# Kernel optimization log

Measured on AMD Instinct MI355X. Metric: run time of the kernel, lower is better.

Reference implementation:

```python
import jax, jax.numpy as jnp
import numpy as np

DIM = 512
HID = 4 * DIM
E = 8
B, T = 2, 2048


def setup_inputs() -> dict:
    key = jax.random.key(0)
    ks = jax.random.split(key, 8)
    s = 0.02
    x = jax.random.normal(ks[0], (B, T, DIM), dtype=jnp.float32)
    route = jax.random.randint(ks[1], (B * T,), 0, E, dtype=jnp.int32)
    # stacked per-expert params; Linear y = x @ W + b with W in [in, out] layout
    w_in = jax.random.normal(ks[2], (E, DIM, HID), dtype=jnp.float32) * s
    b_in = jnp.zeros((E, HID), dtype=jnp.float32)
    w_gate = jax.random.normal(ks[3], (E, DIM, HID), dtype=jnp.float32) * s
    b_gate = jnp.zeros((E, HID), dtype=jnp.float32)
    w_out = jax.random.normal(ks[4], (E, HID, DIM), dtype=jnp.float32) * s
    b_out = jnp.zeros((E, DIM), dtype=jnp.float32)
    return {"x": x, "route": route, "w_in": w_in, "b_in": b_in,
            "w_gate": w_gate, "b_gate": b_gate, "w_out": w_out, "b_out": b_out}


def reference(x, route, w_in, b_in, w_gate, b_gate, w_out, b_out):
    Bb, Tt, C = x.shape
    xf = x.reshape(-1, C)  # [N, C]
    out = jnp.zeros_like(xf)
    n_experts = w_in.shape[0]
    # loop over the small fixed expert set; each expert is a SwiGLU FFN,
    # output scattered back by masking (same math as output[idx] += expert(x[idx]))
    for e in range(n_experts):
        mask = (route == e).astype(xf.dtype)[:, None]  # [N, 1]
        h = jax.nn.silu(xf @ w_gate[e] + b_gate[e]) * (xf @ w_in[e] + b_in[e])  # [N, 4C]
        out = out + mask * (h @ w_out[e] + b_out[e])
    return out.reshape(Bb, Tt, C)
```

## Files before the change

kernel.cpp:

```cpp
#include <hip/hip_runtime.h>

#define DIM 512
#define HID 2048
#define NEXP 8

typedef __attribute__((ext_vector_type(8))) short v8s;
typedef __attribute__((ext_vector_type(4))) float v4f;

__device__ __forceinline__ unsigned short f2bf(float f) {
  union { __bf16 b; unsigned short u; } c;
  c.b = (__bf16)f;
  return c.u;
}

__device__ __forceinline__ void gload16(const void* g, void* l) {
  __builtin_amdgcn_global_load_lds(
      (const __attribute__((address_space(1))) unsigned int*)g,
      (__attribute__((address_space(3))) unsigned int*)l, 16, 0, 0);
}

__global__ void route_prep(const int* __restrict__ route, int* __restrict__ meta, int ntok) {
  __shared__ int c[NEXP];
  int t = threadIdx.x;
  if (t < NEXP) c[t] = 0;
  __syncthreads();
  for (int n = t; n < ntok; n += blockDim.x) atomicAdd(&c[route[n]], 1);
  __syncthreads();
  if (t == 0) {
    int acc = 0, pacc = 0;
    for (int e = 0; e < NEXP; ++e) {
      meta[e] = c[e];
      meta[NEXP + e] = acc;
      meta[2 * NEXP + e] = acc;
      meta[3 * NEXP + e] = pacc;
      acc += c[e];
      pacc += ((c[e] + 127) >> 7) << 7;
    }
  }
}

__global__ void fill_perm(const int* __restrict__ route, int* __restrict__ meta,
                          int* __restrict__ perm, int ntok) {
  int n = blockIdx.x * blockDim.x + threadIdx.x;
  if (n < ntok) {
    int p = atomicAdd(&meta[2 * NEXP + route[n]], 1);
    perm[p] = n;
  }
}

__global__ __launch_bounds__(256) void x_conv(
    const float* __restrict__ x, const int* __restrict__ meta,
    const int* __restrict__ perm, unsigned short* __restrict__ xp)
{
  const int bid = blockIdx.x;
  const int e = bid & 7;
  const int mt = bid >> 3;
  const int cnt = meta[e];
  const int padded = ((cnt + 127) >> 7) << 7;
  if (mt * 64 >= padded) return;
  const int off  = meta[NEXP + e];
  const int poff = meta[3 * NEXP + e];
  const int t = threadIdx.x;
  const int r = t & 63, q = t >> 6;
  int arow = mt * 64 + r; if (arow >= cnt) arow = cnt - 1;
  const float* src = x + (size_t)perm[off + arow] * DIM + q * 128;
  unsigned short* dst = xp + (size_t)((poff + mt * 64) >> 6) * 32768;
  #pragma unroll
  for (int j = 0; j < 16; ++j) {
    float4 f0 = ((const float4*)src)[2 * j];
    float4 f1 = ((const float4*)src)[2 * j + 1];
    v8s v;
    v[0] = (short)f2bf(f0.x); v[1] = (short)f2bf(f0.y);
    v[2] = (short)f2bf(f0.z); v[3] = (short)f2bf(f0.w);
    v[4] = (short)f2bf(f1.x); v[5] = (short)f2bf(f1.y);
    v[6] = (short)f2bf(f1.z); v[7] = (short)f2bf(f1.w);
    *(v8s*)(dst + (size_t)((q * 16 + j) * 64 + r) * 8) = v;
  }
}

__global__ __launch_bounds__(256) void wo_conv(
    const float* __restrict__ wo, unsigned short* __restrict__ wop)
{
  const int s = blockIdx.x;
  const int j = blockIdx.y;
  const int e = blockIdx.z;
  const float* src = wo + (size_t)e * HID * DIM;
  unsigned short* dst = wop + (((size_t)e * 8 + j) * 32 + s) * 4096;
  const int t = threadIdx.x;
  #pragma unroll
  for (int i = 0; i < 2; ++i) {
    const int c = t + 256 * i;
    const int kq = c >> 6, n = c & 63;
    const float* srow = src + (size_t)(s * 64 + kq * 8) * DIM + j * 64 + n;
    v8s r;
    #pragma unroll
    for (int q = 0; q < 8; ++q) r[q] = (short)f2bf(srow[(size_t)q * DIM]);
    *(v8s*)(dst + (size_t)c * 8) = r;
  }
}

__global__ __launch_bounds__(256, 2) void gemm1w(
    const unsigned short* __restrict__ xp,
    const float* __restrict__ wg_, const float* __restrict__ bg_,
    const float* __restrict__ wi_, const float* __restrict__ bi_,
    const int* __restrict__ meta,
    unsigned short* __restrict__ hbuf)
{
  const int bid = blockIdx.x;
  const int e = bid >> 6;
  const int j = bid & 63;
  const int cnt = meta[e];
  const int poff = meta[3 * NEXP + e];
  const int n0 = j * 32;

  __shared__ __align__(16) unsigned char lds[81920];

  const int t = threadIdx.x;
  const int l = t & 63, w = t >> 6;
  const int wm = w >> 1, wn = w & 1;
  const int fr = l & 15, fg = l >> 4;

  {
    const int r0 = t >> 1;
    const int h  = t & 1;
    #pragma unroll
    for (int m = 0; m < 2; ++m) {
      const float* src = (m ? wi_ : wg_) + (size_t)e * DIM * HID + n0 + h * 16;
      unsigned char* slab = lds + m * 32768;
      #pragma unroll
      for (int p = 0; p < 4; ++p) {
        const int r = p * 128 + r0;
        const float* row = src + (size_t)r * HID;
        float f[16];
        #pragma unroll
        for (int q = 0; q < 4; ++q) {
          float4 v = ((const float4*)row)[q];
          f[4*q] = v.x; f[4*q+1] = v.y; f[4*q+2] = v.z; f[4*q+3] = v.w;
        }
        unsigned char* dst = slab + ((r >> 3) * 32 + h * 16) * 16 + (r & 7) * 2;
        #pragma unroll
        for (int nn = 0; nn < 16; ++nn)
          *(unsigned short*)(dst + nn * 16) = f2bf(f[nn]);
      }
    }
  }

  const int c = n0 + wn * 16 + fr;
  const float bgv = bg_[(size_t)e * HID + c];
  const float biv = bi_[(size_t)e * HID + c];

  unsigned char* albuf = lds + 65536;
  const int nmt = (cnt + 127) >> 7;

  for (int mt = 0; mt < nmt; ++mt) {
    const int m0 = mt * 128;
    const int tile0 = (poff + m0) >> 6;

    auto stage_a = [&](int s, int b) {
      unsigned char* base = albuf + b * 8192;
      #pragma unroll
      for (int i = 0; i < 2; ++i) {
        const int s_ = t + 256 * i;
        const int kq = s_ >> 7, mr = s_ & 127;
        gload16(xp + (size_t)(tile0 + (mr >> 6)) * 32768 +
                     ((size_t)(s * 4 + kq) * 64 + (mr & 63)) * 8,
                base + s_ * 16);
      }
    };

    stage_a(0, 0);
    __syncthreads();

    v4f aG[4], aI[4];
    #pragma unroll
    for (int i = 0; i < 4; ++i) {
      aG[i] = (v4f){0.f, 0.f, 0.f, 0.f};
      aI[i] = (v4f){0.f, 0.f, 0.f, 0.f};
    }

    int cur = 0;
    for (int s = 0; s < 16; ++s) {
      if (s < 15) stage_a(s + 1, cur ^ 1);
      const unsigned char* base = albuf + cur * 8192;
      v8s af[4], gf, inf;
      #pragma unroll
      for (int mf = 0; mf < 4; ++mf)
        af[mf] = *(const v8s*)(base + (fg * 128 + wm * 64 + mf * 16 + fr) * 16);
      gf  = *(const v8s*)(lds + (((s * 4 + fg) * 32) + wn * 16 + fr) * 16);
      inf = *(const v8s*)(lds + 32768 + (((s * 4 + fg) * 32) + wn * 16 + fr) * 16);
      #pragma unroll
      for (int mf = 0; mf < 4; ++mf) {
        aG[mf] = __builtin_amdgcn_mfma_f32_16x16x32_bf16(af[mf], gf,  aG[mf], 0, 0, 0);
        aI[mf] = __builtin_amdgcn_mfma_f32_16x16x32_bf16(af[mf], inf, aI[mf], 0, 0, 0);
      }
      __syncthreads();
      cur ^= 1;
    }

    #pragma unroll
    for (int mf = 0; mf < 4; ++mf)
      #pragma unroll
      for (int jj = 0; jj < 4; ++jj) {
        const int r = wm * 64 + mf * 16 + fg * 4 + jj;
        const float g = aG[mf][jj] + bgv;
        const float v = aI[mf][jj] + biv;
        const float hval = g / (1.f + __expf(-g)) * v;
        const int grow = poff + m0 + r;
        hbuf[(size_t)(grow >> 6) * 131072 + ((size_t)(c >> 3) * 64 + (grow & 63)) * 8 + (c & 7)] = f2bf(hval);
      }
  }
}

__global__ __launch_bounds__(256, 4) void gemm2g(
    const unsigned short* __restrict__ hbuf,
    const unsigned short* __restrict__ wop, const float* __restrict__ bo_,
    const int* __restrict__ meta, const int* __restrict__ perm,
    float* __restrict__ out)
{
  const int bid = blockIdx.x;
  const int stripe = bid & 63;
  const int mt = bid >> 6;
  const int e = stripe >> 3, jn = stripe & 7;
  const int cnt = meta[e];
  const int m0 = mt * 64;
  if (m0 >= cnt) return;
  const int off = meta[NEXP + e], poff = meta[3 * NEXP + e];
  const int n0 = jn * 64;

  __shared__ __align__(16) unsigned char lds[32768];

  const int t = threadIdx.x;
  const int l = t & 63, w = t >> 6;
  const int wm = w >> 1, wn = w & 1;
  const int fr = l & 15, fg = l >> 4;

  const unsigned short* pa = hbuf + (size_t)((poff + m0) >> 6) * 131072;
  const unsigned short* pb = wop + ((size_t)e * 8 + jn) * 131072;

  v4f acc[2][2];
  #pragma unroll
  for (int i = 0; i < 2; ++i) {
    acc[i][0] = (v4f){0.f, 0.f, 0.f, 0.f};
    acc[i][1] = (v4f){0.f, 0.f, 0.f, 0.f};
  }

  auto stage = [&](int s, int b) {
    unsigned char* base = lds + b * 16384;
    #pragma unroll
    for (int i = 0; i < 2; ++i) {
      const int c = t + 256 * i;
      gload16(pa + (size_t)s * 4096 + (size_t)c * 8, base + c * 16);
      gload16(pb + (size_t)s * 4096 + (size_t)c * 8, base + 8192 + c * 16);
    }
  };

  stage(0, 0);
  __syncthreads();

  int cur = 0;
  for (int s = 0; s < 32; ++s) {
    if (s < 31) stage(s + 1, cur ^ 1);
    const unsigned char* base = lds + cur * 16384;
    #pragma unroll
    for (int kk = 0; kk < 2; ++kk) {
      v8s af[2], bf[2];
      #pragma unroll
      for (int mf = 0; mf < 2; ++mf)
        af[mf] = *(const v8s*)(base + ((kk * 4 + fg) * 64 + wm * 32 + mf * 16 + fr) * 16);
      #pragma unroll
      for (int nf = 0; nf < 2; ++nf)
        bf[nf] = *(const v8s*)(base + 8192 + ((kk * 4 + fg) * 64 + wn * 32 + nf * 16 + fr) * 16);
      #pragma unroll
      for (int mf = 0; mf < 2; ++mf)
        #pragma unroll
        for (int nf = 0; nf < 2; ++nf)
          acc[mf][nf] = __builtin_amdgcn_mfma_f32_16x16x32_bf16(af[mf], bf[nf], acc[mf][nf], 0, 0, 0);
    }
    __syncthreads();
    cur ^= 1;
  }

  #pragma unroll
  for (int nf = 0; nf < 2; ++nf) {
    const int c = n0 + wn * 32 + nf * 16 + fr;
    const float bo = bo_[(size_t)e * DIM + c];
    #pragma unroll
    for (int mf = 0; mf < 2; ++mf)
      #pragma unroll
      for (int jj = 0; jj < 4; ++jj) {
        const int r = wm * 32 + mf * 16 + fg * 4 + jj;
        if (m0 + r < cnt)
          out[(size_t)perm[off + m0 + r] * DIM + c] = acc[mf][nf][jj] + bo;
      }
  }
}

extern "C" void kernel_launch(void* const* d_in, const int* in_sizes, int n_in,
                              void* d_out, int out_size, void* d_ws, size_t ws_size,
                              hipStream_t stream) {
  const float* x      = (const float*)d_in[0];
  const int*   route  = (const int*)d_in[1];
  const float* w_in   = (const float*)d_in[2];
  const float* b_in   = (const float*)d_in[3];
  const float* w_gate = (const float*)d_in[4];
  const float* b_gate = (const float*)d_in[5];
  const float* w_out  = (const float*)d_in[6];
  const float* b_out  = (const float*)d_in[7];
  float* out = (float*)d_out;

  const int ntok = in_sizes[1];

  int* meta = (int*)d_ws;
  int* perm = (int*)((char*)d_ws + 128);

  unsigned short* xp   = (unsigned short*)((char*)d_ws + 65536);
  unsigned short* wop  = (unsigned short*)((char*)d_ws + 65536 + 5242880);
  unsigned short* hbuf = (unsigned short*)((char*)d_ws + 65536 + 5242880 + 16777216);

  const int MT64 = (ntok + 63) / 64;

  route_prep<<<1, 256, 0, stream>>>(route, meta, ntok);
  fill_perm<<<(ntok + 255) / 256, 256, 0, stream>>>(route, meta, perm, ntok);
  x_conv<<<NEXP * MT64, 256, 0, stream>>>(x, meta, perm, xp);
  gemm1w<<<NEXP * 64, 256, 0, stream>>>(
      xp, w_gate, b_gate, w_in, b_in, meta, hbuf);
  wo_conv<<<dim3(32, 8, 8), 256, 0, stream>>>(w_out, wop);
  gemm2g<<<64 * MT64, 256, 0, stream>>>(
      hbuf, wop, b_out, meta, perm, out);
}
```

Measured before the change: 114.0 us.

## Read activation and weight fragments straight from global memory, dropping LDS staging

Both expert GEMMs stop staging the A operand (and in the second GEMM also the weight tile) through double-buffered LDS with async global-to-LDS loads. Instead each wave loads its MFMA fragments directly from global memory. The first GEMM now gives each wave its own 64-row M strip with both 16-column N fragments and no block barriers. The second GEMM uses 32-row by 32-column per-wave tiles with more blocks and higher occupancy. This removes barrier and LDS traffic but depends on L2/cache hit rates and exposes global load latency without explicit prefetch.

```diff
diff --git a/kernel.cpp b/kernel.cpp
--- a/kernel.cpp
+++ b/kernel.cpp
@@ -11,12 +11,6 @@
   union { __bf16 b; unsigned short u; } c;
   c.b = (__bf16)f;
   return c.u;
-}
-
-__device__ __forceinline__ void gload16(const void* g, void* l) {
-  __builtin_amdgcn_global_load_lds(
-      (const __attribute__((address_space(1))) unsigned int*)g,
-      (__attribute__((address_space(3))) unsigned int*)l, 16, 0, 0);
 }
 
 __global__ void route_prep(const int* __restrict__ route, int* __restrict__ meta, int ntok) {
@@ -99,7 +93,7 @@
   }
 }
 
-__global__ __launch_bounds__(256, 2) void gemm1w(
+__global__ __launch_bounds__(256, 2) void gemm1r2(
     const unsigned short* __restrict__ xp,
     const float* __restrict__ wg_, const float* __restrict__ bg_,
     const float* __restrict__ wi_, const float* __restrict__ bi_,
@@ -111,13 +105,13 @@
   const int j = bid & 63;
   const int cnt = meta[e];
   const int poff = meta[3 * NEXP + e];
+  const int padded = ((cnt + 127) >> 7) << 7;
   const int n0 = j * 32;
 
-  __shared__ __align__(16) unsigned char lds[81920];
+  __shared__ __align__(16) unsigned char lds[65536];
 
   const int t = threadIdx.x;
   const int l = t & 63, w = t >> 6;
-  const int wm = w >> 1, wn = w & 1;
   const int fr = l & 15, fg = l >> 4;
 
   {
@@ -144,98 +138,92 @@
       }
     }
   }
-
-  const int c = n0 + wn * 16 + fr;
-  const float bgv = bg_[(size_t)e * HID + c];
-  const float biv = bi_[(size_t)e * HID + c];
-
-  unsigned char* albuf = lds + 65536;
-  const int nmt = (cnt + 127) >> 7;
-
-  for (int mt = 0; mt < nmt; ++mt) {
-    const int m0 = mt * 128;
-    const int tile0 = (poff + m0) >> 6;
-
-    auto stage_a = [&](int s, int b) {
-      unsigned char* base = albuf + b * 8192;
-      #pragma unroll
-      for (int i = 0; i < 2; ++i) {
-        const int s_ = t + 256 * i;
-        const int kq = s_ >> 7, mr = s_ & 127;
-        gload16(xp + (size_t)(tile0 + (mr >> 6)) * 32768 +
-                     ((size_t)(s * 4 + kq) * 64 + (mr & 63)) * 8,
-                base + s_ * 16);
-      }
-    };
-
-    stage_a(0, 0);
-    __syncthreads();
-
-    v4f aG[4], aI[4];
-    #pragma unroll
-    for (int i = 0; i < 4; ++i) {
-      aG[i] = (v4f){0.f, 0.f, 0.f, 0.f};
-      aI[i] = (v4f){0.f, 0.f, 0.f, 0.f};
+  __syncthreads();
+
+  const float bg0 = bg_[(size_t)e * HID + n0 + fr];
+  const float bg1 = bg_[(size_t)e * HID + n0 + 16 + fr];
+  const float bi0 = bi_[(size_t)e * HID + n0 + fr];
+  const float bi1 = bi_[(size_t)e * HID + n0 + 16 + fr];
+
+  const int tile0 = poff >> 6;
+
+  for (int m0 = w * 64; m0 < padded; m0 += 256) {
+    v4f aG[4][2], aI[4][2];
+    #pragma unroll
+    for (int i = 0; i < 4; ++i)
+      #pragma unroll
+      for (int q = 0; q < 2; ++q) {
+        aG[i][q] = (v4f){0.f, 0.f, 0.f, 0.f};
+        aI[i][q] = (v4f){0.f, 0.f, 0.f, 0.f};
+      }
+
+    for (int s = 0; s < 16; ++s) {
+      v8s af[4];
+      #pragma unroll
+      for (int mf = 0; mf < 4; ++mf) {
+        const int row = m0 + mf * 16 + fr;
+        af[mf] = *(const v8s*)(xp + (size_t)(tile0 + (row >> 6)) * 32768 +
+                               ((size_t)(s * 4 + fg) * 64 + (row & 63)) * 8);
+      }
+      v8s gf[2], inf[2];
+      #pragma unroll
+      for (int nf = 0; nf < 2; ++nf) {
+        gf[nf]  = *(const v8s*)(lds + (((s * 4 + fg) * 32) + nf * 16 + fr) * 16);
+        inf[nf] = *(const v8s*)(lds + 32768 + (((s * 4 + fg) * 32) + nf * 16 + fr) * 16);
+      }
+      #pragma unroll
+      for (int mf = 0; mf < 4; ++mf)
+        #pragma unroll
+        for (int nf = 0; nf < 2; ++nf) {
+          aG[mf][nf] = __builtin_amdgcn_mfma_f32_16x16x32_bf16(af[mf], gf[nf],  aG[mf][nf], 0, 0, 0);
+          aI[mf][nf] = __builtin_amdgcn_mfma_f32_16x16x32_bf16(af[mf], inf[nf], aI[mf][nf], 0, 0, 0);
+        }
     }
 
-    int cur = 0;
-    for (int s = 0; s < 16; ++s) {
-      if (s < 15) stage_a(s + 1, cur ^ 1);
-      const unsigned char* base = albuf + cur * 8192;
-      v8s af[4], gf, inf;
+    #pragma unroll
+    for (int nf = 0; nf < 2; ++nf) {
+      const int c = n0 + nf * 16 + fr;
+      const float bgv = nf ? bg1 : bg0;
+      const float biv = nf ? bi1 : bi0;
       #pragma unroll
       for (int mf = 0; mf < 4; ++mf)
-        af[mf] = *(const v8s*)(base + (fg * 128 + wm * 64 + mf * 16 + fr) * 16);
-      gf  = *(const v8s*)(lds + (((s * 4 + fg) * 32) + wn * 16 + fr) * 16);
-      inf = *(const v8s*)(lds + 32768 + (((s * 4 + fg) * 32) + wn * 16 + fr) * 16);
-      #pragma unroll
-      for (int mf = 0; mf < 4; ++mf) {
-        aG[mf] = __builtin_amdgcn_mfma_f32_16x16x32_bf16(af[mf], gf,  aG[mf], 0, 0, 0);
-        aI[mf] = __builtin_amdgcn_mfma_f32_16x16x32_bf16(af[mf], inf, aI[mf], 0, 0, 0);
-      }
-      __syncthreads();
-      cur ^= 1;
+        #pragma unroll
+        for (int jj = 0; jj < 4; ++jj) {
+          const int grow = poff + m0 + mf * 16 + fg * 4 + jj;
+          const float g = aG[mf][nf][jj] + bgv;
+          const float v = aI[mf][nf][jj] + biv;
+          const float hval = g / (1.f + __expf(-g)) * v;
+          hbuf[(size_t)(grow >> 6) * 131072 + ((size_t)(c >> 3) * 64 + (grow & 63)) * 8 + (c & 7)] = f2bf(hval);
+        }
     }
-
-    #pragma unroll
-    for (int mf = 0; mf < 4; ++mf)
-      #pragma unroll
-      for (int jj = 0; jj < 4; ++jj) {
-        const int r = wm * 64 + mf * 16 + fg * 4 + jj;
-        const float g = aG[mf][jj] + bgv;
-        const float v = aI[mf][jj] + biv;
-        const float hval = g / (1.f + __expf(-g)) * v;
-        const int grow = poff + m0 + r;
-        hbuf[(size_t)(grow >> 6) * 131072 + ((size_t)(c >> 3) * 64 + (grow & 63)) * 8 + (c & 7)] = f2bf(hval);
-      }
-  }
-}
-
-__global__ __launch_bounds__(256, 4) void gemm2g(
+  }
+}
+
+__global__ __launch_bounds__(256, 8) void gemm2r2(
     const unsigned short* __restrict__ hbuf,
     const unsigned short* __restrict__ wop, const float* __restrict__ bo_,
     const int* __restrict__ meta, const int* __restrict__ perm,
     float* __restrict__ out)
 {
   const int bid = blockIdx.x;
-  const int stripe = bid & 63;
-  const int mt = bid >> 6;
-  const int e = stripe >> 3, jn = stripe & 7;
+  const int stripe = bid & 127;
+  const int mt = bid >> 7;
+  const int e = stripe >> 4, jn = stripe & 15;
   const int cnt = meta[e];
-  const int m0 = mt * 64;
-  if (m0 >= cnt) return;
+  const int m0b = mt * 128;
+  if (m0b >= cnt) return;
   const int off = meta[NEXP + e], poff = meta[3 * NEXP + e];
-  const int n0 = jn * 64;
-
-  __shared__ __align__(16) unsigned char lds[32768];
+  const int n0 = jn * 32;
 
   const int t = threadIdx.x;
   const int l = t & 63, w = t >> 6;
-  const int wm = w >> 1, wn = w & 1;
   const int fr = l & 15, fg = l >> 4;
 
-  const unsigned short* pa = hbuf + (size_t)((poff + m0) >> 6) * 131072;
-  const unsigned short* pb = wop + ((size_t)e * 8 + jn) * 131072;
+  const int m0 = m0b + w * 32;
+  const int tile0 = poff >> 6;
+
+  const unsigned short* pb = wop + ((size_t)e * 8 + (jn >> 1)) * 131072;
+  const int nb = (jn & 1) * 32;
 
   v4f acc[2][2];
   #pragma unroll
@@ -244,53 +232,37 @@
     acc[i][1] = (v4f){0.f, 0.f, 0.f, 0.f};
   }
 
-  auto stage = [&](int s, int b) {
-    unsigned char* base = lds + b * 16384;
-    #pragma unroll
-    for (int i = 0; i < 2; ++i) {
-      const int c = t + 256 * i;
-      gload16(pa + (size_t)s * 4096 + (size_t)c * 8, base + c * 16);
-      gload16(pb + (size_t)s * 4096 + (size_t)c * 8, base + 8192 + c * 16);
-    }
-  };
-
-  stage(0, 0);
-  __syncthreads();
-
-  int cur = 0;
-  for (int s = 0; s < 32; ++s) {
-    if (s < 31) stage(s + 1, cur ^ 1);
-    const unsigned char* base = lds + cur * 16384;
-    #pragma unroll
-    for (int kk = 0; kk < 2; ++kk) {
-      v8s af[2], bf[2];
-      #pragma unroll
-      for (int mf = 0; mf < 2; ++mf)
-        af[mf] = *(const v8s*)(base + ((kk * 4 + fg) * 64 + wm * 32 + mf * 16 + fr) * 16);
-      #pragma unroll
-      for (int nf = 0; nf < 2; ++nf)
-        bf[nf] = *(const v8s*)(base + 8192 + ((kk * 4 + fg) * 64 + wn * 32 + nf * 16 + fr) * 16);
-      #pragma unroll
-      for (int mf = 0; mf < 2; ++mf)
-        #pragma unroll
-        for (int nf = 0; nf < 2; ++nf)
-          acc[mf][nf] = __builtin_amdgcn_mfma_f32_16x16x32_bf16(af[mf], bf[nf], acc[mf][nf], 0, 0, 0);
-    }
-    __syncthreads();
-    cur ^= 1;
+  const int row0 = m0 + fr;
+  const int row1 = m0 + 16 + fr;
+  const size_t abase0 = (size_t)(tile0 + (row0 >> 6)) * 131072 + (size_t)(row0 & 63) * 8;
+  const size_t abase1 = (size_t)(tile0 + (row1 >> 6)) * 131072 + (size_t)(row1 & 63) * 8;
+
+  #pragma unroll 4
+  for (int s = 0; s < 64; ++s) {
+    const int kq = s * 4 + fg;
+    v8s a0 = *(const v8s*)(hbuf + abase0 + (size_t)kq * 512);
+    v8s a1 = *(const v8s*)(hbuf + abase1 + (size_t)kq * 512);
+    const size_t boff = (size_t)(s >> 1) * 4096 +
+                        ((size_t)((s & 1) * 4 + fg) * 64 + nb) * 8;
+    v8s b0 = *(const v8s*)(pb + boff + (size_t)fr * 8);
+    v8s b1 = *(const v8s*)(pb + boff + (size_t)(16 + fr) * 8);
+    acc[0][0] = __builtin_amdgcn_mfma_f32_16x16x32_bf16(a0, b0, acc[0][0], 0, 0, 0);
+    acc[0][1] = __builtin_amdgcn_mfma_f32_16x16x32_bf16(a0, b1, acc[0][1], 0, 0, 0);
+    acc[1][0] = __builtin_amdgcn_mfma_f32_16x16x32_bf16(a1, b0, acc[1][0], 0, 0, 0);
+    acc[1][1] = __builtin_amdgcn_mfma_f32_16x16x32_bf16(a1, b1, acc[1][1], 0, 0, 0);
   }
 
   #pragma unroll
   for (int nf = 0; nf < 2; ++nf) {
-    const int c = n0 + wn * 32 + nf * 16 + fr;
+    const int c = n0 + nf * 16 + fr;
     const float bo = bo_[(size_t)e * DIM + c];
     #pragma unroll
     for (int mf = 0; mf < 2; ++mf)
       #pragma unroll
       for (int jj = 0; jj < 4; ++jj) {
-        const int r = wm * 32 + mf * 16 + fg * 4 + jj;
-        if (m0 + r < cnt)
-          out[(size_t)perm[off + m0 + r] * DIM + c] = acc[mf][nf][jj] + bo;
+        const int r = m0 + mf * 16 + fg * 4 + jj;
+        if (r < cnt)
+          out[(size_t)perm[off + r] * DIM + c] = acc[mf][nf][jj] + bo;
       }
   }
 }
@@ -317,14 +289,15 @@
   unsigned short* wop  = (unsigned short*)((char*)d_ws + 65536 + 5242880);
   unsigned short* hbuf = (unsigned short*)((char*)d_ws + 65536 + 5242880 + 16777216);
 
-  const int MT64 = (ntok + 63) / 64;
+  const int MT64  = (ntok + 63) / 64;
+  const int MT128 = (ntok + 127) / 128;
 
   route_prep<<<1, 256, 0, stream>>>(route, meta, ntok);
   fill_perm<<<(ntok + 255) / 256, 256, 0, stream>>>(route, meta, perm, ntok);
   x_conv<<<NEXP * MT64, 256, 0, stream>>>(x, meta, perm, xp);
-  gemm1w<<<NEXP * 64, 256, 0, stream>>>(
+  gemm1r2<<<NEXP * 64, 256, 0, stream>>>(
       xp, w_gate, b_gate, w_in, b_in, meta, hbuf);
   wo_conv<<<dim3(32, 8, 8), 256, 0, stream>>>(w_out, wop);
-  gemm2g<<<64 * MT64, 256, 0, stream>>>(
+  gemm2r2<<<128 * MT128, 256, 0, stream>>>(
       hbuf, wop, b_out, meta, perm, out);
 }
```

New measurement: 182.5 us. 1.6x slower.

## Give each wave independent 32-row M tiles with A loaded directly from global

Applied to the files above, without the earlier changes.

The first GEMM no longer stages token tiles through double-buffered LDS with block-wide barriers. Each wave now owns a 32-row by 32-column tile and reads A fragments straight from global memory, while the weight slab stays resident in LDS. This removes the per-step __syncthreads and lowers LDS use, and each A fragment feeds twice as many MFMAs per load. The cost is uncached-by-LDS global loads in the inner loop that rely on L1/L2 hits, with no prefetch overlap.

```diff
diff --git a/kernel.cpp b/kernel.cpp
--- a/kernel.cpp
+++ b/kernel.cpp
@@ -99,7 +99,7 @@
   }
 }
 
-__global__ __launch_bounds__(256, 2) void gemm1w(
+__global__ __launch_bounds__(256, 2) void gemm1f2(
     const unsigned short* __restrict__ xp,
     const float* __restrict__ wg_, const float* __restrict__ bg_,
     const float* __restrict__ wi_, const float* __restrict__ bi_,
@@ -111,13 +111,13 @@
   const int j = bid & 63;
   const int cnt = meta[e];
   const int poff = meta[3 * NEXP + e];
+  const int padded = ((cnt + 127) >> 7) << 7;
   const int n0 = j * 32;
 
-  __shared__ __align__(16) unsigned char lds[81920];
+  __shared__ __align__(16) unsigned char lds[65536];
 
   const int t = threadIdx.x;
   const int l = t & 63, w = t >> 6;
-  const int wm = w >> 1, wn = w & 1;
   const int fr = l & 15, fg = l >> 4;
 
   {
@@ -144,70 +144,60 @@
       }
     }
   }
-
-  const int c = n0 + wn * 16 + fr;
-  const float bgv = bg_[(size_t)e * HID + c];
-  const float biv = bi_[(size_t)e * HID + c];
-
-  unsigned char* albuf = lds + 65536;
-  const int nmt = (cnt + 127) >> 7;
-
-  for (int mt = 0; mt < nmt; ++mt) {
-    const int m0 = mt * 128;
-    const int tile0 = (poff + m0) >> 6;
-
-    auto stage_a = [&](int s, int b) {
-      unsigned char* base = albuf + b * 8192;
-      #pragma unroll
-      for (int i = 0; i < 2; ++i) {
-        const int s_ = t + 256 * i;
-        const int kq = s_ >> 7, mr = s_ & 127;
-        gload16(xp + (size_t)(tile0 + (mr >> 6)) * 32768 +
-                     ((size_t)(s * 4 + kq) * 64 + (mr & 63)) * 8,
-                base + s_ * 16);
+  __syncthreads();
+
+  const float bg0 = bg_[(size_t)e * HID + n0 + fr];
+  const float bg1 = bg_[(size_t)e * HID + n0 + 16 + fr];
+  const float bi0 = bi_[(size_t)e * HID + n0 + fr];
+  const float bi1 = bi_[(size_t)e * HID + n0 + 16 + fr];
+
+  const int tile0 = poff >> 6;
+
+  for (int m0 = w * 32; m0 < padded; m0 += 128) {
+    const unsigned short* abase = xp + (size_t)(tile0 + (m0 >> 6)) * 32768;
+    const int rb = m0 & 32;
+
+    v4f aG00 = {0,0,0,0}, aG01 = {0,0,0,0}, aG10 = {0,0,0,0}, aG11 = {0,0,0,0};
+    v4f aI00 = {0,0,0,0}, aI01 = {0,0,0,0}, aI10 = {0,0,0,0}, aI11 = {0,0,0,0};
+
+    #pragma unroll 2
+    for (int s = 0; s < 16; ++s) {
+      const int kq = s * 4 + fg;
+      v8s af0 = *(const v8s*)(abase + ((size_t)kq * 64 + rb + fr) * 8);
+      v8s af1 = *(const v8s*)(abase + ((size_t)kq * 64 + rb + 16 + fr) * 8);
+      v8s gf0 = *(const v8s*)(lds + ((kq * 32) + fr) * 16);
+      v8s gf1 = *(const v8s*)(lds + ((kq * 32) + 16 + fr) * 16);
+      v8s if0 = *(const v8s*)(lds + 32768 + ((kq * 32) + fr) * 16);
+      v8s if1 = *(const v8s*)(lds + 32768 + ((kq * 32) + 16 + fr) * 16);
+      aG00 = __builtin_amdgcn_mfma_f32_16x16x32_bf16(af0, gf0, aG00, 0, 0, 0);
+      aG01 = __builtin_amdgcn_mfma_f32_16x16x32_bf16(af0, gf1, aG01, 0, 0, 0);
+      aG10 = __builtin_amdgcn_mfma_f32_16x16x32_bf16(af1, gf0, aG10, 0, 0, 0);
+      aG11 = __builtin_amdgcn_mfma_f32_16x16x32_bf16(af1, gf1, aG11, 0, 0, 0);
+      aI00 = __builtin_amdgcn_mfma_f32_16x16x32_bf16(af0, if0, aI00, 0, 0, 0);
+      aI01 = __builtin_amdgcn_mfma_f32_16x16x32_bf16(af0, if1, aI01, 0, 0, 0);
+      aI10 = __builtin_amdgcn_mfma_f32_16x16x32_bf16(af1, if0, aI10, 0, 0, 0);
+      aI11 = __builtin_amdgcn_mfma_f32_16x16x32_bf16(af1, if1, aI11, 0, 0, 0);
+    }
+
+    #pragma unroll
+    for (int nf = 0; nf < 2; ++nf) {
+      const int c = n0 + nf * 16 + fr;
+      const float bgv = nf ? bg1 : bg0;
+      const float biv = nf ? bi1 : bi0;
+      #pragma unroll
+      for (int mf = 0; mf < 2; ++mf) {
+        const v4f g4 = nf ? (mf ? aG11 : aG01) : (mf ? aG10 : aG00);
+        const v4f i4 = nf ? (mf ? aI11 : aI01) : (mf ? aI10 : aI00);
+        #pragma unroll
+        for (int jj = 0; jj < 4; ++jj) {
+          const int grow = poff + m0 + mf * 16 + fg * 4 + jj;
+          const float g = g4[jj] + bgv;
+          const float v = i4[jj] + biv;
+          const float hval = g / (1.f + __expf(-g)) * v;
+          hbuf[(size_t)(grow >> 6) * 131072 + ((size_t)(c >> 3) * 64 + (grow & 63)) * 8 + (c & 7)] = f2bf(hval);
+        }
       }
-    };
-
-    stage_a(0, 0);
-    __syncthreads();
-
-    v4f aG[4], aI[4];
-    #pragma unroll
-    for (int i = 0; i < 4; ++i) {
-      aG[i] = (v4f){0.f, 0.f, 0.f, 0.f};
-      aI[i] = (v4f){0.f, 0.f, 0.f, 0.f};
-    }
-
-    int cur = 0;
-    for (int s = 0; s < 16; ++s) {
-      if (s < 15) stage_a(s + 1, cur ^ 1);
-      const unsigned char* base = albuf + cur * 8192;
-      v8s af[4], gf, inf;
-      #pragma unroll
-      for (int mf = 0; mf < 4; ++mf)
-        af[mf] = *(const v8s*)(base + (fg * 128 + wm * 64 + mf * 16 + fr) * 16);
-      gf  = *(const v8s*)(lds + (((s * 4 + fg) * 32) + wn * 16 + fr) * 16);
-      inf = *(const v8s*)(lds + 32768 + (((s * 4 + fg) * 32) + wn * 16 + fr) * 16);
-      #pragma unroll
-      for (int mf = 0; mf < 4; ++mf) {
-        aG[mf] = __builtin_amdgcn_mfma_f32_16x16x32_bf16(af[mf], gf,  aG[mf], 0, 0, 0);
-        aI[mf] = __builtin_amdgcn_mfma_f32_16x16x32_bf16(af[mf], inf, aI[mf], 0, 0, 0);
-      }
-      __syncthreads();
-      cur ^= 1;
-    }
-
-    #pragma unroll
-    for (int mf = 0; mf < 4; ++mf)
-      #pragma unroll
-      for (int jj = 0; jj < 4; ++jj) {
-        const int r = wm * 64 + mf * 16 + fg * 4 + jj;
-        const float g = aG[mf][jj] + bgv;
-        const float v = aI[mf][jj] + biv;
-        const float hval = g / (1.f + __expf(-g)) * v;
-        const int grow = poff + m0 + r;
-        hbuf[(size_t)(grow >> 6) * 131072 + ((size_t)(c >> 3) * 64 + (grow & 63)) * 8 + (c & 7)] = f2bf(hval);
-      }
+    }
   }
 }
 
@@ -322,7 +312,7 @@
   route_prep<<<1, 256, 0, stream>>>(route, meta, ntok);
   fill_perm<<<(ntok + 255) / 256, 256, 0, stream>>>(route, meta, perm, ntok);
   x_conv<<<NEXP * MT64, 256, 0, stream>>>(x, meta, perm, xp);
-  gemm1w<<<NEXP * 64, 256, 0, stream>>>(
+  gemm1f2<<<NEXP * 64, 256, 0, stream>>>(
       xp, w_gate, b_gate, w_in, b_in, meta, hbuf);
   wo_conv<<<dim3(32, 8, 8), 256, 0, stream>>>(w_out, wop);
   gemm2g<<<64 * MT64, 256, 0, stream>>>(
```

New measurement: 113.8 us. Within noise of the previous version (-0.2%).
